# Performance work log

Measured on AMD Instinct MI355X. Metric: run time of the kernel, lower is better.

Reference implementation:

```python
import jax, jax.numpy as jnp
import numpy as np

NUM_HEADS = 8
AGENT_NUM = 49
POOL = 7


def _pool_matrix(in_size, out_size):
    # adaptive average pool weights, matches torch AdaptiveAvgPool2d binning
    P = np.zeros((out_size, in_size), np.float32)
    for i in range(out_size):
        s = (i * in_size) // out_size
        e = -((-(i + 1) * in_size) // out_size)
        P[i, s:e] = 1.0 / (e - s)
    return jnp.asarray(P)


def _conv2d(x, w, b, groups=1):
    y = jax.lax.conv_general_dilated(
        x, w, window_strides=(1, 1), padding='SAME',
        dimension_numbers=('NCHW', 'OIHW', 'NCHW'), feature_group_count=groups)
    return y + b[None, :, None, None]


def setup_inputs() -> dict:
    key = jax.random.key(0)
    ks = jax.random.split(key, 16)
    b, n, dim, inner, ctx = 16, 4096, 512, 512, 256
    H = W = cH = cW = 64
    inp = {
        'x': jax.random.normal(ks[0], (b, n, dim), jnp.float32),
        'context': jax.random.normal(ks[1], (b, cH * cW, ctx), jnp.float32),
        'q_w': jax.random.normal(ks[2], (inner, dim), jnp.float32) * 0.02,
        'kv_w': jax.random.normal(ks[3], (2 * inner, dim), jnp.float32) * 0.02,
        'proj_w': jax.random.normal(ks[4], (dim, inner), jnp.float32) * 0.02,
        'proj_b': jax.random.normal(ks[5], (dim,), jnp.float32) * 0.02,
        'conv_w': jax.random.normal(ks[6], (inner, inner + ctx, 3, 3), jnp.float32) * 0.02,
        'conv_b': jax.random.normal(ks[7], (inner,), jnp.float32) * 0.02,
        'dwc_w': jax.random.normal(ks[8], (inner, 1, 3, 3), jnp.float32) * 0.02,
        'dwc_b': jax.random.normal(ks[9], (inner,), jnp.float32) * 0.02,
        'an_bias': jax.random.normal(ks[10], (NUM_HEADS, AGENT_NUM, 7, 7), jnp.float32) * 0.02,
        'na_bias': jax.random.normal(ks[11], (NUM_HEADS, AGENT_NUM, 7, 7), jnp.float32) * 0.02,
        'ah_bias': jax.random.normal(ks[12], (1, NUM_HEADS, AGENT_NUM, H, 1), jnp.float32) * 0.02,
        'aw_bias': jax.random.normal(ks[13], (1, NUM_HEADS, AGENT_NUM, 1, W), jnp.float32) * 0.02,
        'ha_bias': jax.random.normal(ks[14], (1, NUM_HEADS, H, 1, AGENT_NUM), jnp.float32) * 0.02,
        'wa_bias': jax.random.normal(ks[15], (1, NUM_HEADS, 1, W, AGENT_NUM), jnp.float32) * 0.02,
        'H': H, 'W': W, 'c_H': cH, 'c_W': cW,
    }
    return inp


def reference(x, context, q_w, kv_w, proj_w, proj_b, conv_w, conv_b, dwc_w, dwc_b,
              an_bias, na_bias, ah_bias, aw_bias, ha_bias, wa_bias, H, W, c_H, c_W):
    b, n, c = x.shape
    heads, agent_num = NUM_HEADS, AGENT_NUM
    inner = q_w.shape[0]
    ctx_c = context.shape[-1]
    hd = inner // heads
    scale = hd ** (-0.5)

    q = x @ q_w.T                                   # (b, n, inner)
    kv = x @ kv_w.T                                 # (b, n, 2*inner)
    k, v = kv[..., :inner], kv[..., inner:]

    # agent tokens: adaptive-avg-pool q and context to 7x7, concat, 3x3 conv
    Ph, Pw = _pool_matrix(H, POOL), _pool_matrix(W, POOL)
    Pch, Pcw = _pool_matrix(c_H, POOL), _pool_matrix(c_W, POOL)
    pool_x = jnp.einsum('ph,qw,bhwc->bpqc', Ph, Pw, q.reshape(b, H, W, inner)).reshape(b, POOL * POOL, inner)
    pool_ctx = jnp.einsum('ph,qw,bhwc->bpqc', Pch, Pcw, context.reshape(b, c_H, c_W, ctx_c)).reshape(b, POOL * POOL, ctx_c)
    # NOTE: raw reshape (b,49,C)->(b,C,7,7), faithful to the torch code
    agent = jnp.concatenate([pool_x, pool_ctx], axis=2).reshape(b, inner + ctx_c, POOL, POOL)
    agent = _conv2d(agent, conv_w, conv_b).reshape(b, inner, agent_num)
    agent = agent.reshape(b, agent_num, heads, hd).transpose(0, 2, 1, 3)   # (b,h,a,d)

    qh = q.reshape(b, n, heads, hd).transpose(0, 2, 1, 3)  # (b,h,n,d)
    kh = k.reshape(b, n, heads, hd).transpose(0, 2, 1, 3)
    vh = v.reshape(b, n, heads, hd).transpose(0, 2, 1, 3)

    # stage 1: agent -> kv attention
    pb1 = jax.image.resize(an_bias, (heads, agent_num, H, W), method='bilinear').reshape(1, heads, agent_num, n)
    pb2 = (ah_bias + aw_bias).reshape(1, heads, agent_num, n)
    agent_attn = jax.nn.softmax(jnp.einsum('bhad,bhnd->bhan', agent * scale, kh) + pb1 + pb2, axis=-1)
    agent_v = jnp.einsum('bhan,bhnd->bhad', agent_attn, vh)

    # stage 2: query -> agent attention
    ab1 = jax.image.resize(na_bias, (heads, agent_num, H, W), method='bilinear').reshape(1, heads, agent_num, n).transpose(0, 1, 3, 2)
    ab2 = (ha_bias + wa_bias).reshape(1, heads, n, agent_num)
    q_attn = jax.nn.softmax(jnp.einsum('bhnd,bhad->bhna', qh * scale, agent) + ab1 + ab2, axis=-1)
    out = jnp.einsum('bhna,bhad->bhnd', q_attn, agent_v).transpose(0, 2, 1, 3).reshape(b, n, inner)

    # depthwise conv residual on v
    v_img = vh.transpose(0, 2, 1, 3).reshape(b, H, W, inner).transpose(0, 3, 1, 2)
    out = out + _conv2d(v_img, dwc_w, dwc_b, groups=inner).transpose(0, 2, 3, 1).reshape(b, n, inner)

    return out @ proj_w.T + proj_b
```

## Files before the change

### kernel.cpp

```cpp
#include <hip/hip_runtime.h>
#include <cstdint>
#include <cstddef>

#define BB    16
#define NTOK  4096
#define DIMC  512
#define INNER 512
#define CTXC  256
#define HEADS 8
#define HD    64
#define AG    49
#define ASPLIT 8
#define CONVK 6912
#define CKS   16

static const size_t Q_OFF   = 0;
static const size_t KV_OFF  = Q_OFF  + (size_t)BB*NTOK*INNER;
static const size_t A2_OFF  = KV_OFF + (size_t)BB*NTOK*2*INNER;
static const size_t COL_OFF = A2_OFF + (size_t)BB*AG*768;
static const size_t CG_OFF  = COL_OFF+ (size_t)BB*AG*768*9;
static const size_t AGT_OFF = CG_OFF + (size_t)BB*AG*INNER;
static const size_t AGV_OFF = AGT_OFF+ (size_t)BB*HEADS*AG*HD;
static const size_t PB_OFF  = AGV_OFF+ (size_t)BB*HEADS*AG*HD;
static const size_t AB_OFF  = PB_OFF + (size_t)HEADS*AG*NTOK;
static const size_t WSP_OFF = AB_OFF + (size_t)HEADS*NTOK*AG;
static const size_t PNUM_OFF = COL_OFF;
static const size_t PL_OFF   = PNUM_OFF + (size_t)ASPLIT*128*64*64;
static const size_t AVT_OFF  = PL_OFF + (size_t)ASPLIT*128*64;

typedef __attribute__((ext_vector_type(8))) short  short8;
typedef __attribute__((ext_vector_type(8))) __bf16 bf16x8;
typedef __attribute__((ext_vector_type(4))) float  f32x4;

union SB8 { short8 s; bf16x8 b; };

__device__ inline bf16x8 asbf(short8 v) { SB8 u; u.s = v; return u.b; }

__device__ inline unsigned short bfrn(float x) {
  uint32_t u = __float_as_uint(x);
  return (unsigned short)((u + 0x7FFFu + ((u >> 16) & 1u)) >> 16);
}

struct HL8 { short8 h, l; };

__device__ inline HL8 split8(float4 f0, float4 f1) {
  HL8 r;
  float v0[4] = {f0.x, f0.y, f0.z, f0.w};
  float v1[4] = {f1.x, f1.y, f1.z, f1.w};
#pragma unroll
  for (int j = 0; j < 4; ++j) {
    unsigned short hb = bfrn(v0[j]);
    r.h[j] = (short)hb;
    r.l[j] = (short)bfrn(v0[j] - __uint_as_float((uint32_t)hb << 16));
  }
#pragma unroll
  for (int j = 0; j < 4; ++j) {
    unsigned short hb = bfrn(v1[j]);
    r.h[j + 4] = (short)hb;
    r.l[j + 4] = (short)bfrn(v1[j] - __uint_as_float((uint32_t)hb << 16));
  }
  return r;
}

__device__ inline HL8 split8t(float4 f0, float4 f1) {
  HL8 r;
  float v[8] = {f0.x, f0.y, f0.z, f0.w, f1.x, f1.y, f1.z, f1.w};
#pragma unroll
  for (int j = 0; j < 8; ++j) {
    uint32_t u = __float_as_uint(v[j]);
    uint32_t hb = (u + 0x7FFFu + ((u >> 16) & 1u)) >> 16;
    r.h[j] = (short)hb;
    float res = v[j] - __uint_as_float(hb << 16);
    r.l[j] = (short)(__float_as_uint(res) >> 16);
  }
  return r;
}

__global__ void split_w_kernel(const float* __restrict__ src, short* __restrict__ dhi,
                               short* __restrict__ dlo, int n8) {
  int i = blockIdx.x * 256 + threadIdx.x;
  if (i >= n8) return;
  const float4* s = (const float4*)src + (size_t)i * 2;
  HL8 r = split8(s[0], s[1]);
  *(short8*)(dhi + (size_t)i * 8) = r.h;
  *(short8*)(dlo + (size_t)i * 8) = r.l;
}

#define LSTR 40
template <bool ADD_BIAS>
__global__ __launch_bounds__(256) void gemm_ws3(const float* __restrict__ A,
                                                const short* __restrict__ Bhi_g,
                                                const short* __restrict__ Blo_g,
                                                const float* __restrict__ bias,
                                                float* __restrict__ C1, int nc1,
                                                float* __restrict__ C2, int nc2,
                                                int M, int K) {
  __shared__ short Ahi[128 * LSTR];
  __shared__ short Alo[128 * LSTR];
  __shared__ short Bhi[128 * LSTR];
  __shared__ short Blo[128 * LSTR];
  const int tid  = threadIdx.x;
  const int lane = tid & 63;
  const int wave = tid >> 6;
  const int wm = wave >> 1, wn = wave & 1;
  const int nwg = gridDim.x * gridDim.y;
  const int lin = blockIdx.y * gridDim.x + blockIdx.x;
  const int swz = (lin & 7) * (nwg >> 3) + (lin >> 3);
  const int bx = swz % gridDim.x, by = swz / gridDim.x;
  const int bm = by * 128, bnT = bx * 128;
  const int srow  = tid >> 1;
  const int shalf = (tid & 1) << 4;
  const int fr  = lane & 15;
  const int fko = (lane >> 4) << 3;

  f32x4 acc[4][4] = {};

  for (int k0 = 0; k0 < K; k0 += 32) {
    {
      const float4* ap = (const float4*)(A + (size_t)(bm + srow) * K + k0 + shalf);
      float4 a0 = ap[0], a1 = ap[1], a2 = ap[2], a3 = ap[3];
      HL8 r0 = split8t(a0, a1);
      *(short8*)&Ahi[srow * LSTR + shalf] = r0.h;
      *(short8*)&Alo[srow * LSTR + shalf] = r0.l;
      HL8 r1 = split8t(a2, a3);
      *(short8*)&Ahi[srow * LSTR + shalf + 8] = r1.h;
      *(short8*)&Alo[srow * LSTR + shalf + 8] = r1.l;
      const short* bhp = Bhi_g + (size_t)(bnT + srow) * K + k0 + shalf;
      *(short8*)&Bhi[srow * LSTR + shalf]     = *(const short8*)bhp;
      *(short8*)&Bhi[srow * LSTR + shalf + 8] = *(const short8*)(bhp + 8);
      const short* blp = Blo_g + (size_t)(bnT + srow) * K + k0 + shalf;
      *(short8*)&Blo[srow * LSTR + shalf]     = *(const short8*)blp;
      *(short8*)&Blo[srow * LSTR + shalf + 8] = *(const short8*)(blp + 8);
    }
    __syncthreads();
    bf16x8 ah[4], al[4], bh[4], bl[4];
#pragma unroll
    for (int i = 0; i < 4; ++i) {
      int ra = wm * 64 + i * 16 + fr;
      ah[i] = asbf(*(const short8*)&Ahi[ra * LSTR + fko]);
      al[i] = asbf(*(const short8*)&Alo[ra * LSTR + fko]);
      int rb = wn * 64 + i * 16 + fr;
      bh[i] = asbf(*(const short8*)&Bhi[rb * LSTR + fko]);
      bl[i] = asbf(*(const short8*)&Blo[rb * LSTR + fko]);
    }
#pragma unroll
    for (int i = 0; i < 4; ++i)
#pragma unroll
      for (int j = 0; j < 4; ++j) {
        acc[i][j] = __builtin_amdgcn_mfma_f32_16x16x32_bf16(ah[i], bh[j], acc[i][j], 0, 0, 0);
        acc[i][j] = __builtin_amdgcn_mfma_f32_16x16x32_bf16(ah[i], bl[j], acc[i][j], 0, 0, 0);
        acc[i][j] = __builtin_amdgcn_mfma_f32_16x16x32_bf16(al[i], bh[j], acc[i][j], 0, 0, 0);
      }
    __syncthreads();
  }

  const int crow0 = wm * 64 + ((lane >> 4) << 2);
  const int ccol0 = wn * 64 + fr;
  float* Cb; int ncb, coff;
  if (bnT < nc1) { Cb = C1; ncb = nc1; coff = bnT; }
  else           { Cb = C2; ncb = nc2; coff = bnT - nc1; }
  float bs[4];
  if (ADD_BIAS) {
#pragma unroll
    for (int j = 0; j < 4; ++j) bs[j] = bias[bnT + ccol0 + j * 16];
  }
#pragma unroll
  for (int i = 0; i < 4; ++i) {
#pragma unroll
    for (int r = 0; r < 4; ++r) {
      size_t row = (size_t)(bm + crow0 + i * 16 + r);
      float* cp = Cb + row * ncb + coff + ccol0;
#pragma unroll
      for (int j = 0; j < 4; ++j) {
        float v = acc[i][j][r];
        if (ADD_BIAS) v += bs[j];
        cp[j * 16] = v;
      }
    }
  }
}

__global__ void zero_kernel(float* __restrict__ p, int n) {
  int i = blockIdx.x * 256 + threadIdx.x;
  if (i < n) p[i] = 0.f;
}

__global__ __launch_bounds__(256) void conv_gemm_splitk(const float* __restrict__ A,
                                                        const float* __restrict__ Bw,
                                                        float* __restrict__ C) {
  __shared__ float As[16][72];
  __shared__ float Bs[16][72];
  const int tid = threadIdx.x;
  const int tx = tid & 15, ty = tid >> 4;
  const int bn = blockIdx.x * 64;
  const int bm = blockIdx.y * 64;
  const int k_begin = blockIdx.z * (CONVK / CKS);
  const int k_end = k_begin + (CONVK / CKS);
  const int row = tid >> 2, c4 = (tid & 3) << 2;
  float acc[4][4] = {};
  for (int k0 = k_begin; k0 < k_end; k0 += 16) {
    {
      int m = bm + row;
      float4 av = {0.f, 0.f, 0.f, 0.f};
      if (m < 784) av = *(const float4*)(A + (size_t)m * CONVK + k0 + c4);
      As[c4 + 0][row] = av.x; As[c4 + 1][row] = av.y;
      As[c4 + 2][row] = av.z; As[c4 + 3][row] = av.w;
      float4 bv = *(const float4*)(Bw + (size_t)(bn + row) * CONVK + k0 + c4);
      Bs[c4 + 0][row] = bv.x; Bs[c4 + 1][row] = bv.y;
      Bs[c4 + 2][row] = bv.z; Bs[c4 + 3][row] = bv.w;
    }
    __syncthreads();
#pragma unroll
    for (int k = 0; k < 16; ++k) {
      float a[4], b[4];
#pragma unroll
      for (int i = 0; i < 4; ++i) a[i] = As[k][ty * 4 + i];
#pragma unroll
      for (int j = 0; j < 4; ++j) b[j] = Bs[k][tx * 4 + j];
#pragma unroll
      for (int i = 0; i < 4; ++i)
#pragma unroll
        for (int j = 0; j < 4; ++j) acc[i][j] = fmaf(a[i], b[j], acc[i][j]);
    }
    __syncthreads();
  }
#pragma unroll
  for (int i = 0; i < 4; ++i) {
    int m = bm + ty * 4 + i;
    if (m >= 784) continue;
#pragma unroll
    for (int j = 0; j < 4; ++j)
      atomicAdd(C + (size_t)m * INNER + bn + tx * 4 + j, acc[i][j]);
  }
}

__global__ void pool_h_kernel(const float* __restrict__ q, const float* __restrict__ ctx,
                              float* __restrict__ S1q, float* __restrict__ S1c) {
  int idx = blockIdx.x * 256 + threadIdx.x;
  if (idx >= BB * 7 * 64 * 768) return;
  int c  = idx % 768;
  int w  = (idx / 768) & 63;
  int ph = (idx / (768 * 64)) % 7;
  int b  = idx / (768 * 64 * 7);
  int hs = ph * 64 / 7, he = ((ph + 1) * 64 + 6) / 7;
  float s = 0.f;
  if (c < 512) {
    const float* p = q + ((size_t)b * NTOK + hs * 64 + w) * INNER + c;
    for (int h = hs; h < he; ++h) { s += *p; p += 64 * INNER; }
    S1q[((size_t)(b * 7 + ph) * 64 + w) * 512 + c] = s;
  } else {
    int cc = c - 512;
    const float* p = ctx + ((size_t)b * NTOK + hs * 64 + w) * CTXC + cc;
    for (int h = hs; h < he; ++h) { s += *p; p += 64 * CTXC; }
    S1c[((size_t)(b * 7 + ph) * 64 + w) * 256 + cc] = s;
  }
}

__global__ void pool_w_kernel(const float* __restrict__ S1q, const float* __restrict__ S1c,
                              float* __restrict__ A2) {
  int idx = blockIdx.x * 256 + threadIdx.x;
  if (idx >= BB * AG * 768) return;
  int c = idx % 768;
  int p = (idx / 768) % AG;
  int b = idx / (768 * AG);
  int i = p / 7, j = p % 7;
  int hs = i * 64 / 7, he = ((i + 1) * 64 + 6) / 7;
  int ws = j * 64 / 7, we = ((j + 1) * 64 + 6) / 7;
  float inv = 1.f / (float)((he - hs) * (we - ws));
  float s = 0.f;
  if (c < 512) {
    const float* pp = S1q + ((size_t)(b * 7 + i) * 64 + ws) * 512 + c;
    for (int w = ws; w < we; ++w) { s += *pp; pp += 512; }
  } else {
    const float* pp = S1c + ((size_t)(b * 7 + i) * 64 + ws) * 256 + (c - 512);
    for (int w = ws; w < we; ++w) { s += *pp; pp += 256; }
  }
  A2[((size_t)b * AG + p) * 768 + c] = s * inv;
}

__global__ void im2col_kernel(const float* __restrict__ A2, float* __restrict__ Col) {
  int idx = blockIdx.x * 256 + threadIdx.x;
  if (idx >= 784 * 6912) return;
  int r = idx / 6912, t = idx % 6912;
  int ic = t / 9, ky = (t % 9) / 3, kx = t % 3;
  int b = r / AG, p = r % AG;
  int y = p / 7 + ky - 1, x = p % 7 + kx - 1;
  float v = 0.f;
  if (y >= 0 && y < 7 && x >= 0 && x < 7) {
    int g = ic * 49 + y * 7 + x;
    v = A2[((size_t)b * AG + g / 768) * 768 + (g % 768)];
  }
  Col[(size_t)idx] = v;
}

__global__ void agent_scatter_kernel(const float* __restrict__ Cg, const float* __restrict__ conv_b,
                                     float* __restrict__ agent) {
  int idx = blockIdx.x * 256 + threadIdx.x;
  if (idx >= BB * HEADS * AG * HD) return;
  int d = idx & 63;
  int a = (idx >> 6) % AG;
  int h = (idx / (64 * AG)) % HEADS;
  int b = idx / (64 * AG * HEADS);
  int f = a * 512 + h * 64 + d;
  int oc = f / 49, p = f % 49;
  agent[idx] = Cg[((size_t)b * AG + p) * INNER + oc] + conv_b[oc];
}

__device__ inline float bilinear7(const float* __restrict__ Bm, int y, int x) {
  float fy = (y + 0.5f) * (7.f / 64.f) - 0.5f;
  float fx = (x + 0.5f) * (7.f / 64.f) - 0.5f;
  fy = fminf(fmaxf(fy, 0.f), 6.f);
  fx = fminf(fmaxf(fx, 0.f), 6.f);
  int y0 = min((int)floorf(fy), 5);
  int x0 = min((int)floorf(fx), 5);
  float ty = fy - y0, tx = fx - x0;
  float v00 = Bm[y0 * 7 + x0],     v01 = Bm[y0 * 7 + x0 + 1];
  float v10 = Bm[(y0 + 1) * 7 + x0], v11 = Bm[(y0 + 1) * 7 + x0 + 1];
  return (1.f - ty) * ((1.f - tx) * v00 + tx * v01) + ty * ((1.f - tx) * v10 + tx * v11);
}

__global__ void pb_kernel(const float* __restrict__ an_bias, const float* __restrict__ ah,
                          const float* __restrict__ aw, float* __restrict__ pb) {
  int idx = blockIdx.x * 256 + threadIdx.x;
  if (idx >= HEADS * AG * NTOK) return;
  int nn = idx & (NTOK - 1);
  int a = (idx / NTOK) % AG;
  int h = idx / (NTOK * AG);
  int y = nn >> 6, x = nn & 63;
  float v = bilinear7(an_bias + ((size_t)h * AG + a) * 49, y, x);
  v += ah[((size_t)h * AG + a) * 64 + y] + aw[((size_t)h * AG + a) * 64 + x];
  pb[idx] = v;
}

__global__ void ab_kernel(const float* __restrict__ na_bias, const float* __restrict__ ha,
                          const float* __restrict__ wa, float* __restrict__ ab) {
  int idx = blockIdx.x * 256 + threadIdx.x;
  if (idx >= HEADS * NTOK * AG) return;
  int a = idx % AG;
  int nn = (idx / AG) & (NTOK - 1);
  int h = idx / (AG * NTOK);
  int y = nn >> 6, x = nn & 63;
  float v = bilinear7(na_bias + ((size_t)h * AG + a) * 49, y, x);
  v += ha[((size_t)h * 64 + y) * AG + a] + wa[((size_t)h * 64 + x) * AG + a];
  ab[idx] = v;
}

__global__ __launch_bounds__(256, 2) void agent_attn_s(const float* __restrict__ kv,
                                                       const float* __restrict__ agent,
                                                       const float* __restrict__ pb,
                                                       float* __restrict__ part_num,
                                                       float* __restrict__ part_l) {
  const int split = blockIdx.x;
  const int h = blockIdx.y, b = blockIdx.z;
  const int bh = b * HEADS + h;
  __shared__ float agT[64][68];
  __shared__ float ktT[64][68];
  __shared__ float vt[64][68];
  __shared__ float eT[64][68];
  const int tid = threadIdx.x;
  const int tx = tid & 15, ty = tid >> 4;

  for (int idx = tid; idx < AG * 16; idx += 256) {
    int a = idx >> 4, d0 = (idx & 15) << 2;
    float4 v4 = *(const float4*)(agent + ((size_t)bh * AG + a) * HD + d0);
    agT[d0 + 0][a] = v4.x * 0.125f; agT[d0 + 1][a] = v4.y * 0.125f;
    agT[d0 + 2][a] = v4.z * 0.125f; agT[d0 + 3][a] = v4.w * 0.125f;
  }
  for (int idx = tid; idx < 64 * 15; idx += 256) {
    int d = idx / 15, a = AG + idx % 15;
    agT[d][a] = 0.f;
  }

  float accR[4][4] = {};
  float lR[4] = {};

  const float* kb = kv + (size_t)b * NTOK * 1024 + h * 64;
  const float* vb = kb + 512;
  const float* pbh = pb + (size_t)h * AG * NTOK;

  const int nrow = tid & 63, dq = tid >> 6;

  for (int c = 0; c < 8; ++c) {
    const int n0 = split * 512 + c * 64;
#pragma unroll
    for (int i = 0; i < 4; ++i) {
      int d = dq * 16 + i * 4;
      float4 kk = *(const float4*)(kb + (size_t)(n0 + nrow) * 1024 + d);
      ktT[d + 0][nrow] = kk.x; ktT[d + 1][nrow] = kk.y;
      ktT[d + 2][nrow] = kk.z; ktT[d + 3][nrow] = kk.w;
      float4 vv = *(const float4*)(vb + (size_t)(n0 + nrow) * 1024 + d);
      *(float4*)&vt[nrow][d] = vv;
    }
    __syncthreads();
    float s[4][4] = {};
#pragma unroll 4
    for (int d = 0; d < 64; ++d) {
      float4 a4 = *(float4*)&agT[d][ty * 4];
      float4 k4 = *(float4*)&ktT[d][tx * 4];
      s[0][0] = fmaf(a4.x, k4.x, s[0][0]); s[0][1] = fmaf(a4.x, k4.y, s[0][1]);
      s[0][2] = fmaf(a4.x, k4.z, s[0][2]); s[0][3] = fmaf(a4.x, k4.w, s[0][3]);
      s[1][0] = fmaf(a4.y, k4.x, s[1][0]); s[1][1] = fmaf(a4.y, k4.y, s[1][1]);
      s[1][2] = fmaf(a4.y, k4.z, s[1][2]); s[1][3] = fmaf(a4.y, k4.w, s[1][3]);
      s[2][0] = fmaf(a4.z, k4.x, s[2][0]); s[2][1] = fmaf(a4.z, k4.y, s[2][1]);
      s[2][2] = fmaf(a4.z, k4.z, s[2][2]); s[2][3] = fmaf(a4.z, k4.w, s[2][3]);
      s[3][0] = fmaf(a4.w, k4.x, s[3][0]); s[3][1] = fmaf(a4.w, k4.y, s[3][1]);
      s[3][2] = fmaf(a4.w, k4.z, s[3][2]); s[3][3] = fmaf(a4.w, k4.w, s[3][3]);
    }
#pragma unroll
    for (int i = 0; i < 4; ++i) {
      int a = ty * 4 + i;
      int ac = a < AG ? a : AG - 1;
      float4 p4 = *(const float4*)(pbh + (size_t)ac * NTOK + n0 + tx * 4);
      float e0 = __expf(s[i][0] + p4.x);
      float e1 = __expf(s[i][1] + p4.y);
      float e2 = __expf(s[i][2] + p4.z);
      float e3 = __expf(s[i][3] + p4.w);
      lR[i] += e0 + e1 + e2 + e3;
      eT[tx * 4 + 0][a] = e0; eT[tx * 4 + 1][a] = e1;
      eT[tx * 4 + 2][a] = e2; eT[tx * 4 + 3][a] = e3;
    }
    __syncthreads();
#pragma unroll 4
    for (int n = 0; n < 64; ++n) {
      float4 e4 = *(float4*)&eT[n][ty * 4];
      float4 v4 = *(float4*)&vt[n][tx * 4];
      accR[0][0] = fmaf(e4.x, v4.x, accR[0][0]); accR[0][1] = fmaf(e4.x, v4.y, accR[0][1]);
      accR[0][2] = fmaf(e4.x, v4.z, accR[0][2]); accR[0][3] = fmaf(e4.x, v4.w, accR[0][3]);
      accR[1][0] = fmaf(e4.y, v4.x, accR[1][0]); accR[1][1] = fmaf(e4.y, v4.y, accR[1][1]);
      accR[1][2] = fmaf(e4.y, v4.z, accR[1][2]); accR[1][3] = fmaf(e4.y, v4.w, accR[1][3]);
      accR[2][0] = fmaf(e4.z, v4.x, accR[2][0]); accR[2][1] = fmaf(e4.z, v4.y, accR[2][1]);
      accR[2][2] = fmaf(e4.z, v4.z, accR[2][2]); accR[2][3] = fmaf(e4.z, v4.w, accR[2][3]);
      accR[3][0] = fmaf(e4.w, v4.x, accR[3][0]); accR[3][1] = fmaf(e4.w, v4.y, accR[3][1]);
      accR[3][2] = fmaf(e4.w, v4.z, accR[3][2]); accR[3][3] = fmaf(e4.w, v4.w, accR[3][3]);
    }
    __syncthreads();
  }
#pragma unroll
  for (int i = 0; i < 4; ++i) {
    float l = lR[i];
    l += __shfl_xor(l, 1, 64); l += __shfl_xor(l, 2, 64);
    l += __shfl_xor(l, 4, 64); l += __shfl_xor(l, 8, 64);
    lR[i] = l;
  }
  float* pn = part_num + ((size_t)(split * 128 + bh)) * 64 * 64;
  float* pl = part_l + (size_t)(split * 128 + bh) * 64;
#pragma unroll
  for (int i = 0; i < 4; ++i) {
    int a = ty * 4 + i;
    if (a < AG) {
      float4 o = {accR[i][0], accR[i][1], accR[i][2], accR[i][3]};
      *(float4*)(pn + a * 64 + tx * 4) = o;
      if (tx == 0) pl[a] = lR[i];
    }
  }
}

__global__ void agent_attn_combine(const float* __restrict__ part_num,
                                   const float* __restrict__ part_l,
                                   short* __restrict__ avThi, short* __restrict__ avTlo) {
  int idx = blockIdx.x * 256 + threadIdx.x;
  if (idx >= 128 * 64 * 64) return;
  int a = idx & 63;
  int d = (idx >> 6) & 63;
  int bh = idx >> 12;
  float v = 0.f;
  if (a < AG) {
    float num = 0.f, l = 0.f;
#pragma unroll
    for (int s = 0; s < ASPLIT; ++s) {
      num += part_num[((size_t)(s * 128 + bh)) * 4096 + a * 64 + d];
      l += part_l[(size_t)(s * 128 + bh) * 64 + a];
    }
    v = num / l;
  }
  unsigned short hb = bfrn(v);
  float res = v - __uint_as_float((uint32_t)hb << 16);
  avThi[(size_t)bh * 4096 + d * 64 + a] = (short)hb;
  avTlo[(size_t)bh * 4096 + d * 64 + a] = (short)(__float_as_uint(res) >> 16);
}

#define PSTR 80
__global__ __launch_bounds__(256) void q_attn_mfma(const float* __restrict__ agent,
                                                   const short* __restrict__ avThi,
                                                   const short* __restrict__ avTlo,
                                                   const float* __restrict__ ab,
                                                   float* __restrict__ q) {
  const int tile = blockIdx.x;
  const int h = blockIdx.y, b = blockIdx.z;
  const int bh = b * HEADS + h;
  __shared__ short Phi[128 * PSTR];
  __shared__ short Plo[128 * PSTR];
  const int tid = threadIdx.x;
  const int lane = tid & 63;
  const int wave = tid >> 6;
  const int woff = wave * 32;
  const int fr = lane & 15;
  const int fko = (lane >> 4) << 3;
  const int rg = lane >> 4;

  const size_t agbase = (size_t)bh * AG * HD;
  const int gtok0 = tile * 128 + woff;
  const size_t qrow0 = (size_t)b * NTOK + gtok0;

  bf16x8 agh[2][4], agl[2][4];
#pragma unroll
  for (int j = 0; j < 4; ++j) {
    int ar = j * 16 + fr; if (ar > AG - 1) ar = AG - 1;
#pragma unroll
    for (int kh = 0; kh < 2; ++kh) {
      const float4* p = (const float4*)(agent + agbase + (size_t)ar * HD + kh * 32 + fko);
      float4 f0 = p[0], f1 = p[1];
      f0.x *= 0.125f; f0.y *= 0.125f; f0.z *= 0.125f; f0.w *= 0.125f;
      f1.x *= 0.125f; f1.y *= 0.125f; f1.z *= 0.125f; f1.w *= 0.125f;
      HL8 r = split8t(f0, f1);
      agh[kh][j] = asbf(r.h); agl[kh][j] = asbf(r.l);
    }
  }

  bf16x8 qh_[2][2], ql_[2][2];
#pragma unroll
  for (int i = 0; i < 2; ++i)
#pragma unroll
    for (int kh = 0; kh < 2; ++kh) {
      const float4* p = (const float4*)(q + (qrow0 + i * 16 + fr) * INNER + h * 64 + kh * 32 + fko);
      HL8 r = split8t(p[0], p[1]);
      qh_[i][kh] = asbf(r.h); ql_[i][kh] = asbf(r.l);
    }

  f32x4 sa[2][4] = {};
#pragma unroll
  for (int i = 0; i < 2; ++i)
#pragma unroll
    for (int j = 0; j < 4; ++j)
#pragma unroll
      for (int kh = 0; kh < 2; ++kh) {
        sa[i][j] = __builtin_amdgcn_mfma_f32_16x16x32_bf16(qh_[i][kh], agh[kh][j], sa[i][j], 0, 0, 0);
        sa[i][j] = __builtin_amdgcn_mfma_f32_16x16x32_bf16(qh_[i][kh], agl[kh][j], sa[i][j], 0, 0, 0);
        sa[i][j] = __builtin_amdgcn_mfma_f32_16x16x32_bf16(ql_[i][kh], agh[kh][j], sa[i][j], 0, 0, 0);
      }

  float ev[2][4][4];
  float lsum[2][4];
#pragma unroll
  for (int i = 0; i < 2; ++i) {
#pragma unroll
    for (int r = 0; r < 4; ++r) {
      int t = gtok0 + i * 16 + 4 * rg + r;
      const float* abp = ab + ((size_t)h * NTOK + t) * AG;
      float sv[4];
      float m = -3.4e38f;
#pragma unroll
      for (int j = 0; j < 4; ++j) {
        int a = j * 16 + fr;
        int ac = a < AG ? a : AG - 1;
        float xv = sa[i][j][r] + abp[ac];
        sv[j] = (a < AG) ? xv : -3.4e38f;
        m = fmaxf(m, sv[j]);
      }
      m = fmaxf(m, __shfl_xor(m, 1, 64));
      m = fmaxf(m, __shfl_xor(m, 2, 64));
      m = fmaxf(m, __shfl_xor(m, 4, 64));
      m = fmaxf(m, __shfl_xor(m, 8, 64));
      float l = 0.f;
#pragma unroll
      for (int j = 0; j < 4; ++j) {
        int a = j * 16 + fr;
        float e = (a < AG) ? __expf(sv[j] - m) : 0.f;
        ev[i][j][r] = e;
        l += e;
      }
      l += __shfl_xor(l, 1, 64);
      l += __shfl_xor(l, 2, 64);
      l += __shfl_xor(l, 4, 64);
      l += __shfl_xor(l, 8, 64);
      lsum[i][r] = l;
    }
  }

#pragma unroll
  for (int i = 0; i < 2; ++i)
#pragma unroll
    for (int r = 0; r < 4; ++r) {
      int lt = woff + i * 16 + 4 * rg + r;
#pragma unroll
      for (int j = 0; j < 4; ++j) {
        int a = j * 16 + fr;
        float e = ev[i][j][r];
        unsigned short hb = bfrn(e);
        float res = e - __uint_as_float((uint32_t)hb << 16);
        Phi[lt * PSTR + a] = (short)hb;
        Plo[lt * PSTR + a] = (short)(__float_as_uint(res) >> 16);
      }
    }
  __syncthreads();

  const short* avhp = avThi + (size_t)bh * 4096;
  const short* avlp = avTlo + (size_t)bh * 4096;
  bf16x8 vh_[2][4], vl_[2][4];
#pragma unroll
  for (int j = 0; j < 4; ++j)
#pragma unroll
    for (int kh = 0; kh < 2; ++kh) {
      size_t o = (size_t)(j * 16 + fr) * 64 + kh * 32 + fko;
      vh_[kh][j] = asbf(*(const short8*)(avhp + o));
      vl_[kh][j] = asbf(*(const short8*)(avlp + o));
    }
  bf16x8 ph_[2][2], pl_[2][2];
#pragma unroll
  for (int i = 0; i < 2; ++i)
#pragma unroll
    for (int kh = 0; kh < 2; ++kh) {
      int lt = woff + i * 16 + fr;
      ph_[i][kh] = asbf(*(const short8*)&Phi[lt * PSTR + kh * 32 + fko]);
      pl_[i][kh] = asbf(*(const short8*)&Plo[lt * PSTR + kh * 32 + fko]);
    }
  f32x4 oa[2][4] = {};
#pragma unroll
  for (int i = 0; i < 2; ++i)
#pragma unroll
    for (int j = 0; j < 4; ++j)
#pragma unroll
      for (int kh = 0; kh < 2; ++kh) {
        oa[i][j] = __builtin_amdgcn_mfma_f32_16x16x32_bf16(ph_[i][kh], vh_[kh][j], oa[i][j], 0, 0, 0);
        oa[i][j] = __builtin_amdgcn_mfma_f32_16x16x32_bf16(ph_[i][kh], vl_[kh][j], oa[i][j], 0, 0, 0);
        oa[i][j] = __builtin_amdgcn_mfma_f32_16x16x32_bf16(pl_[i][kh], vh_[kh][j], oa[i][j], 0, 0, 0);
      }

#pragma unroll
  for (int i = 0; i < 2; ++i)
#pragma unroll
    for (int r = 0; r < 4; ++r) {
      float inv = 1.f / lsum[i][r];
      float* qp = q + (qrow0 + i * 16 + 4 * rg + r) * INNER + h * 64;
#pragma unroll
      for (int j = 0; j < 4; ++j)
        qp[j * 16 + fr] = oa[i][j][r] * inv;
    }
}

__global__ __launch_bounds__(256) void dwc4_kernel(const float* __restrict__ kv,
                                                   const float* __restrict__ dwc_w,
                                                   const float* __restrict__ dwc_b,
                                                   float* __restrict__ outp) {
  int idx = blockIdx.x * 256 + threadIdx.x;
  int cq = (idx & 127) << 2;
  int r  = idx >> 7;
  int x = r & 63, y = (r >> 6) & 63, b = r >> 12;
  float wreg[36];
  {
    const float4* wp = (const float4*)(dwc_w + (size_t)cq * 9);
#pragma unroll
    for (int j = 0; j < 9; ++j) {
      float4 t = wp[j];
      wreg[4 * j + 0] = t.x; wreg[4 * j + 1] = t.y;
      wreg[4 * j + 2] = t.z; wreg[4 * j + 3] = t.w;
    }
  }
  float4 s = *(const float4*)(dwc_b + cq);
  const float* vb = kv + (size_t)b * NTOK * 1024 + 512 + cq;
#pragma unroll
  for (int ky = 0; ky < 3; ++ky) {
    int yy = y + ky - 1;
    if (yy < 0 || yy > 63) continue;
#pragma unroll
    for (int kx = 0; kx < 3; ++kx) {
      int xx = x + kx - 1;
      if (xx < 0 || xx > 63) continue;
      float4 v4 = *(const float4*)(vb + (size_t)(yy * 64 + xx) * 1024);
      const int t = ky * 3 + kx;
      s.x = fmaf(wreg[0 * 9 + t], v4.x, s.x);
      s.y = fmaf(wreg[1 * 9 + t], v4.y, s.y);
      s.z = fmaf(wreg[2 * 9 + t], v4.z, s.z);
      s.w = fmaf(wreg[3 * 9 + t], v4.w, s.w);
    }
  }
  size_t o = (size_t)r * INNER + cq;
  float4 cur = *(const float4*)(outp + o);
  cur.x += s.x; cur.y += s.y; cur.z += s.z; cur.w += s.w;
  *(float4*)(outp + o) = cur;
}

extern "C" void kernel_launch(void* const* d_in, const int* in_sizes, int n_in,
                              void* d_out, int out_size, void* d_ws, size_t ws_size,
                              hipStream_t stream) {
  const float* x       = (const float*)d_in[0];
  const float* context = (const float*)d_in[1];
  const float* q_w     = (const float*)d_in[2];
  const float* kv_w    = (const float*)d_in[3];
  const float* proj_w  = (const float*)d_in[4];
  const float* proj_b  = (const float*)d_in[5];
  const float* conv_w  = (const float*)d_in[6];
  const float* conv_b  = (const float*)d_in[7];
  const float* dwc_w   = (const float*)d_in[8];
  const float* dwc_b   = (const float*)d_in[9];
  const float* an_bias = (const float*)d_in[10];
  const float* na_bias = (const float*)d_in[11];
  const float* ah_bias = (const float*)d_in[12];
  const float* aw_bias = (const float*)d_in[13];
  const float* ha_bias = (const float*)d_in[14];
  const float* wa_bias = (const float*)d_in[15];
  float* out = (float*)d_out;
  float* wsf = (float*)d_ws;

  float* q_buf  = wsf + Q_OFF;
  float* kv_buf = wsf + KV_OFF;
  float* A2     = wsf + A2_OFF;
  float* Col    = wsf + COL_OFF;
  float* Cg     = wsf + CG_OFF;
  float* agent  = wsf + AGT_OFF;
  float* pb     = wsf + PB_OFF;
  float* ab     = wsf + AB_OFF;
  float* pnum   = wsf + PNUM_OFF;
  float* pl     = wsf + PL_OFF;
  short* avThi  = (short*)(wsf + AVT_OFF);
  short* avTlo  = avThi + (size_t)128 * 64 * 64;
  short* whi    = (short*)(wsf + WSP_OFF);
  short* wlo    = whi + (size_t)2048 * 512;
  float* S1q    = wsf + COL_OFF;
  float* S1c    = wsf + CG_OFF;

  const int M = BB * NTOK;

  split_w_kernel<<<(512 * 512 / 8 + 255) / 256, 256, 0, stream>>>(q_w, whi, wlo, 512 * 512 / 8);
  split_w_kernel<<<(1024 * 512 / 8 + 255) / 256, 256, 0, stream>>>(kv_w, whi + (size_t)512 * 512, wlo + (size_t)512 * 512, 1024 * 512 / 8);
  split_w_kernel<<<(512 * 512 / 8 + 255) / 256, 256, 0, stream>>>(proj_w, whi + (size_t)1536 * 512, wlo + (size_t)1536 * 512, 512 * 512 / 8);

  gemm_ws3<false><<<dim3(1536 / 128, M / 128), 256, 0, stream>>>(x, whi, wlo, nullptr,
                                                                 q_buf, INNER, kv_buf, 2 * INNER, M, DIMC);
  pool_h_kernel<<<(BB * 7 * 64 * 768) / 256, 256, 0, stream>>>(q_buf, context, S1q, S1c);
  pool_w_kernel<<<(BB * AG * 768 + 255) / 256, 256, 0, stream>>>(S1q, S1c, A2);
  im2col_kernel<<<(784 * 6912 + 255) / 256, 256, 0, stream>>>(A2, Col);
  zero_kernel<<<(784 * INNER + 255) / 256, 256, 0, stream>>>(Cg, 784 * INNER);
  conv_gemm_splitk<<<dim3(INNER / 64, (784 + 63) / 64, CKS), 256, 0, stream>>>(Col, conv_w, Cg);
  agent_scatter_kernel<<<(BB * HEADS * AG * HD + 255) / 256, 256, 0, stream>>>(Cg, conv_b, agent);
  pb_kernel<<<(HEADS * AG * NTOK + 255) / 256, 256, 0, stream>>>(an_bias, ah_bias, aw_bias, pb);
  ab_kernel<<<(HEADS * NTOK * AG + 255) / 256, 256, 0, stream>>>(na_bias, ha_bias, wa_bias, ab);
  agent_attn_s<<<dim3(ASPLIT, HEADS, BB), 256, 0, stream>>>(kv_buf, agent, pb, pnum, pl);
  agent_attn_combine<<<(128 * 64 * 64) / 256, 256, 0, stream>>>(pnum, pl, avThi, avTlo);
  q_attn_mfma<<<dim3(NTOK / 128, HEADS, BB), 256, 0, stream>>>(agent, avThi, avTlo, ab, q_buf);
  dwc4_kernel<<<(BB * NTOK * 128) / 256, 256, 0, stream>>>(kv_buf, dwc_w, dwc_b, q_buf);
  gemm_ws3<true><<<dim3(DIMC / 128, M / 128), 256, 0, stream>>>(q_buf, whi + (size_t)1536 * 512, wlo + (size_t)1536 * 512,
                                                                proj_b, out, DIMC, out, 0, M, INNER);

  (void)in_sizes; (void)n_in; (void)out_size; (void)ws_size;
}
```

Measured before the change: 1.434 ms.

## Port agent-to-kv attention stage to split-bf16 MFMA matrix instructions

Replaces the scalar-FMA agent attention kernel with one that computes agent·K scores and exp(scores)·V on MFMA 16x16x32 bf16 instructions. Operands are split into hi/lo bf16 pairs and multiplied with three MFMAs to keep near-fp32 accuracy. K fragments load straight into registers, while V and the exponentials are staged transposed in LDS as bf16 hi/lo. This cuts ALU cost for a kernel that reads all of K and V, at the cost of split-conversion work, scalar pb loads and strided LDS stores.

```diff
diff --git a/kernel.cpp b/kernel.cpp
--- a/kernel.cpp
+++ b/kernel.cpp
@@ -345,114 +345,150 @@
   ab[idx] = v;
 }
 
-__global__ __launch_bounds__(256, 2) void agent_attn_s(const float* __restrict__ kv,
-                                                       const float* __restrict__ agent,
-                                                       const float* __restrict__ pb,
-                                                       float* __restrict__ part_num,
-                                                       float* __restrict__ part_l) {
+#define ESTR 72
+__global__ __launch_bounds__(256, 2) void agent_attn_mfma(const float* __restrict__ kv,
+                                                          const float* __restrict__ agent,
+                                                          const float* __restrict__ pb,
+                                                          float* __restrict__ part_num,
+                                                          float* __restrict__ part_l) {
   const int split = blockIdx.x;
   const int h = blockIdx.y, b = blockIdx.z;
   const int bh = b * HEADS + h;
-  __shared__ float agT[64][68];
-  __shared__ float ktT[64][68];
-  __shared__ float vt[64][68];
-  __shared__ float eT[64][68];
+  __shared__ short eThi[64 * ESTR];
+  __shared__ short eTlo[64 * ESTR];
+  __shared__ short vThi[64 * ESTR];
+  __shared__ short vTlo[64 * ESTR];
+  __shared__ float lred[4][64];
   const int tid = threadIdx.x;
-  const int tx = tid & 15, ty = tid >> 4;
-
-  for (int idx = tid; idx < AG * 16; idx += 256) {
-    int a = idx >> 4, d0 = (idx & 15) << 2;
-    float4 v4 = *(const float4*)(agent + ((size_t)bh * AG + a) * HD + d0);
-    agT[d0 + 0][a] = v4.x * 0.125f; agT[d0 + 1][a] = v4.y * 0.125f;
-    agT[d0 + 2][a] = v4.z * 0.125f; agT[d0 + 3][a] = v4.w * 0.125f;
-  }
-  for (int idx = tid; idx < 64 * 15; idx += 256) {
-    int d = idx / 15, a = AG + idx % 15;
-    agT[d][a] = 0.f;
-  }
-
-  float accR[4][4] = {};
-  float lR[4] = {};
+  const int lane = tid & 63;
+  const int w = tid >> 6;
+  const int fr = lane & 15;
+  const int fko = (lane >> 4) << 3;
+  const int rg = lane >> 4;
+
+  bf16x8 agh[4][2], agl[4][2];
+#pragma unroll
+  for (int i = 0; i < 4; ++i) {
+    int ar = i * 16 + fr; if (ar > AG - 1) ar = AG - 1;
+#pragma unroll
+    for (int kh = 0; kh < 2; ++kh) {
+      const float4* p = (const float4*)(agent + ((size_t)bh * AG + ar) * HD + kh * 32 + fko);
+      float4 f0 = p[0], f1 = p[1];
+      f0.x *= 0.125f; f0.y *= 0.125f; f0.z *= 0.125f; f0.w *= 0.125f;
+      f1.x *= 0.125f; f1.y *= 0.125f; f1.z *= 0.125f; f1.w *= 0.125f;
+      HL8 r = split8t(f0, f1);
+      agh[i][kh] = asbf(r.h); agl[i][kh] = asbf(r.l);
+    }
+  }
+
+  float lacc[4][4] = {};
+  f32x4 oa[4] = {};
 
   const float* kb = kv + (size_t)b * NTOK * 1024 + h * 64;
   const float* vb = kb + 512;
   const float* pbh = pb + (size_t)h * AG * NTOK;
-
   const int nrow = tid & 63, dq = tid >> 6;
 
   for (int c = 0; c < 8; ++c) {
     const int n0 = split * 512 + c * 64;
-#pragma unroll
-    for (int i = 0; i < 4; ++i) {
-      int d = dq * 16 + i * 4;
-      float4 kk = *(const float4*)(kb + (size_t)(n0 + nrow) * 1024 + d);
-      ktT[d + 0][nrow] = kk.x; ktT[d + 1][nrow] = kk.y;
-      ktT[d + 2][nrow] = kk.z; ktT[d + 3][nrow] = kk.w;
-      float4 vv = *(const float4*)(vb + (size_t)(n0 + nrow) * 1024 + d);
-      *(float4*)&vt[nrow][d] = vv;
-    }
+    {
+      const float* vr = vb + (size_t)(n0 + nrow) * 1024;
+#pragma unroll
+      for (int p = 0; p < 2; ++p) {
+        int d0 = dq * 16 + p * 8;
+        float4 f0 = *(const float4*)(vr + d0);
+        float4 f1 = *(const float4*)(vr + d0 + 4);
+        HL8 r = split8t(f0, f1);
+#pragma unroll
+        for (int j = 0; j < 8; ++j) {
+          vThi[(d0 + j) * ESTR + nrow] = r.h[j];
+          vTlo[(d0 + j) * ESTR + nrow] = r.l[j];
+        }
+      }
+    }
+    bf16x8 kh_[2], kl_[2];
+    {
+      const float* kr = kb + (size_t)(n0 + w * 16 + fr) * 1024;
+#pragma unroll
+      for (int kh = 0; kh < 2; ++kh) {
+        float4 f0 = *(const float4*)(kr + kh * 32 + fko);
+        float4 f1 = *(const float4*)(kr + kh * 32 + fko + 4);
+        HL8 r = split8t(f0, f1);
+        kh_[kh] = asbf(r.h); kl_[kh] = asbf(r.l);
+      }
+    }
+    f32x4 sa[4] = {};
+#pragma unroll
+    for (int i = 0; i < 4; ++i)
+#pragma unroll
+      for (int kh = 0; kh < 2; ++kh) {
+        sa[i] = __builtin_amdgcn_mfma_f32_16x16x32_bf16(agh[i][kh], kh_[kh], sa[i], 0, 0, 0);
+        sa[i] = __builtin_amdgcn_mfma_f32_16x16x32_bf16(agh[i][kh], kl_[kh], sa[i], 0, 0, 0);
+        sa[i] = __builtin_amdgcn_mfma_f32_16x16x32_bf16(agl[i][kh], kh_[kh], sa[i], 0, 0, 0);
+      }
+    const int ncol = n0 + w * 16 + fr;
+#pragma unroll
+    for (int i = 0; i < 4; ++i)
+#pragma unroll
+      for (int r = 0; r < 4; ++r) {
+        int a = i * 16 + 4 * rg + r;
+        float e = 0.f;
+        if (a < AG) e = __expf(sa[i][r] + pbh[(size_t)a * NTOK + ncol]);
+        lacc[i][r] += e;
+        uint32_t u = __float_as_uint(e);
+        uint32_t hb = (u + 0x7FFFu + ((u >> 16) & 1u)) >> 16;
+        float res = e - __uint_as_float(hb << 16);
+        eThi[a * ESTR + w * 16 + fr] = (short)hb;
+        eTlo[a * ESTR + w * 16 + fr] = (short)(__float_as_uint(res) >> 16);
+      }
     __syncthreads();
-    float s[4][4] = {};
-#pragma unroll 4
-    for (int d = 0; d < 64; ++d) {
-      float4 a4 = *(float4*)&agT[d][ty * 4];
-      float4 k4 = *(float4*)&ktT[d][tx * 4];
-      s[0][0] = fmaf(a4.x, k4.x, s[0][0]); s[0][1] = fmaf(a4.x, k4.y, s[0][1]);
-      s[0][2] = fmaf(a4.x, k4.z, s[0][2]); s[0][3] = fmaf(a4.x, k4.w, s[0][3]);
-      s[1][0] = fmaf(a4.y, k4.x, s[1][0]); s[1][1] = fmaf(a4.y, k4.y, s[1][1]);
-      s[1][2] = fmaf(a4.y, k4.z, s[1][2]); s[1][3] = fmaf(a4.y, k4.w, s[1][3]);
-      s[2][0] = fmaf(a4.z, k4.x, s[2][0]); s[2][1] = fmaf(a4.z, k4.y, s[2][1]);
-      s[2][2] = fmaf(a4.z, k4.z, s[2][2]); s[2][3] = fmaf(a4.z, k4.w, s[2][3]);
-      s[3][0] = fmaf(a4.w, k4.x, s[3][0]); s[3][1] = fmaf(a4.w, k4.y, s[3][1]);
-      s[3][2] = fmaf(a4.w, k4.z, s[3][2]); s[3][3] = fmaf(a4.w, k4.w, s[3][3]);
-    }
-#pragma unroll
-    for (int i = 0; i < 4; ++i) {
-      int a = ty * 4 + i;
-      int ac = a < AG ? a : AG - 1;
-      float4 p4 = *(const float4*)(pbh + (size_t)ac * NTOK + n0 + tx * 4);
-      float e0 = __expf(s[i][0] + p4.x);
-      float e1 = __expf(s[i][1] + p4.y);
-      float e2 = __expf(s[i][2] + p4.z);
-      float e3 = __expf(s[i][3] + p4.w);
-      lR[i] += e0 + e1 + e2 + e3;
-      eT[tx * 4 + 0][a] = e0; eT[tx * 4 + 1][a] = e1;
-      eT[tx * 4 + 2][a] = e2; eT[tx * 4 + 3][a] = e3;
-    }
+    bf16x8 vh_[2], vl_[2];
+#pragma unroll
+    for (int kh = 0; kh < 2; ++kh) {
+      vh_[kh] = asbf(*(const short8*)&vThi[(w * 16 + fr) * ESTR + kh * 32 + fko]);
+      vl_[kh] = asbf(*(const short8*)&vTlo[(w * 16 + fr) * ESTR + kh * 32 + fko]);
+    }
+#pragma unroll
+    for (int i = 0; i < 4; ++i)
+#pragma unroll
+      for (int kh = 0; kh < 2; ++kh) {
+        bf16x8 eh = asbf(*(const short8*)&eThi[(i * 16 + fr) * ESTR + kh * 32 + fko]);
+        bf16x8 el = asbf(*(const short8*)&eTlo[(i * 16 + fr) * ESTR + kh * 32 + fko]);
+        oa[i] = __builtin_amdgcn_mfma_f32_16x16x32_bf16(eh, vh_[kh], oa[i], 0, 0, 0);
+        oa[i] = __builtin_amdgcn_mfma_f32_16x16x32_bf16(eh, vl_[kh], oa[i], 0, 0, 0);
+        oa[i] = __builtin_amdgcn_mfma_f32_16x16x32_bf16(el, vh_[kh], oa[i], 0, 0, 0);
+      }
     __syncthreads();
-#pragma unroll 4
-    for (int n = 0; n < 64; ++n) {
-      float4 e4 = *(float4*)&eT[n][ty * 4];
-      float4 v4 = *(float4*)&vt[n][tx * 4];
-      accR[0][0] = fmaf(e4.x, v4.x, accR[0][0]); accR[0][1] = fmaf(e4.x, v4.y, accR[0][1]);
-      accR[0][2] = fmaf(e4.x, v4.z, accR[0][2]); accR[0][3] = fmaf(e4.x, v4.w, accR[0][3]);
-      accR[1][0] = fmaf(e4.y, v4.x, accR[1][0]); accR[1][1] = fmaf(e4.y, v4.y, accR[1][1]);
-      accR[1][2] = fmaf(e4.y, v4.z, accR[1][2]); accR[1][3] = fmaf(e4.y, v4.w, accR[1][3]);
-      accR[2][0] = fmaf(e4.z, v4.x, accR[2][0]); accR[2][1] = fmaf(e4.z, v4.y, accR[2][1]);
-      accR[2][2] = fmaf(e4.z, v4.z, accR[2][2]); accR[2][3] = fmaf(e4.z, v4.w, accR[2][3]);
-      accR[3][0] = fmaf(e4.w, v4.x, accR[3][0]); accR[3][1] = fmaf(e4.w, v4.y, accR[3][1]);
-      accR[3][2] = fmaf(e4.w, v4.z, accR[3][2]); accR[3][3] = fmaf(e4.w, v4.w, accR[3][3]);
-    }
-    __syncthreads();
-  }
-#pragma unroll
-  for (int i = 0; i < 4; ++i) {
-    float l = lR[i];
-    l += __shfl_xor(l, 1, 64); l += __shfl_xor(l, 2, 64);
-    l += __shfl_xor(l, 4, 64); l += __shfl_xor(l, 8, 64);
-    lR[i] = l;
-  }
+  }
+
+#pragma unroll
+  for (int i = 0; i < 4; ++i)
+#pragma unroll
+    for (int r = 0; r < 4; ++r) {
+      float l = lacc[i][r];
+      l += __shfl_xor(l, 1, 64); l += __shfl_xor(l, 2, 64);
+      l += __shfl_xor(l, 4, 64); l += __shfl_xor(l, 8, 64);
+      lacc[i][r] = l;
+    }
+  if (fr == 0) {
+#pragma unroll
+    for (int i = 0; i < 4; ++i)
+#pragma unroll
+      for (int r = 0; r < 4; ++r)
+        lred[w][i * 16 + 4 * rg + r] = lacc[i][r];
+  }
+  __syncthreads();
+
   float* pn = part_num + ((size_t)(split * 128 + bh)) * 64 * 64;
   float* pl = part_l + (size_t)(split * 128 + bh) * 64;
 #pragma unroll
-  for (int i = 0; i < 4; ++i) {
-    int a = ty * 4 + i;
-    if (a < AG) {
-      float4 o = {accR[i][0], accR[i][1], accR[i][2], accR[i][3]};
-      *(float4*)(pn + a * 64 + tx * 4) = o;
-      if (tx == 0) pl[a] = lR[i];
-    }
-  }
+  for (int i = 0; i < 4; ++i)
+#pragma unroll
+    for (int r = 0; r < 4; ++r) {
+      int a = i * 16 + 4 * rg + r;
+      if (a < AG) pn[a * 64 + w * 16 + fr] = oa[i][r];
+    }
+  if (tid < AG) pl[tid] = lred[0][tid] + lred[1][tid] + lred[2][tid] + lred[3][tid];
 }
 
 __global__ void agent_attn_combine(const float* __restrict__ part_num,
@@ -735,7 +771,7 @@
   agent_scatter_kernel<<<(BB * HEADS * AG * HD + 255) / 256, 256, 0, stream>>>(Cg, conv_b, agent);
   pb_kernel<<<(HEADS * AG * NTOK + 255) / 256, 256, 0, stream>>>(an_bias, ah_bias, aw_bias, pb);
   ab_kernel<<<(HEADS * NTOK * AG + 255) / 256, 256, 0, stream>>>(na_bias, ha_bias, wa_bias, ab);
-  agent_attn_s<<<dim3(ASPLIT, HEADS, BB), 256, 0, stream>>>(kv_buf, agent, pb, pnum, pl);
+  agent_attn_mfma<<<dim3(ASPLIT, HEADS, BB), 256, 0, stream>>>(kv_buf, agent, pb, pnum, pl);
   agent_attn_combine<<<(128 * 64 * 64) / 256, 256, 0, stream>>>(pnum, pl, avThi, avTlo);
   q_attn_mfma<<<dim3(NTOK / 128, HEADS, BB), 256, 0, stream>>>(agent, avThi, avTlo, ab, q_buf);
   dwc4_kernel<<<(BB * NTOK * 128) / 256, 256, 0, stream>>>(kv_buf, dwc_w, dwc_b, q_buf);
```

Result: faster. 1.370 ms (-4.5%).
